# Optimization experiments

Hardware: AMD Instinct MI355X
Metric: run time of the kernel (lower is better)

The kernel has to match this reference:

```python
import jax, jax.numpy as jnp
import numpy as np

H = 8          # num_heads
D = 64         # out_dim per head
ROT = D // 2   # rotary dim per spatial axis (out_dim // relative_emb_dim)
MIN_FREQ = 1.0 / 64


def _freqs(t):
    # t: (bs, N) coordinates -> (bs, N, ROT)
    inv_freq = 1.0 / (10000.0 ** (jnp.arange(0, ROT, 2, dtype=jnp.float32) / ROT))
    f = (t / MIN_FREQ)[..., None] * inv_freq  # (bs, N, ROT/2)
    return jnp.concatenate([f, f], axis=-1)   # (bs, N, ROT)


def _rotate_half(x):
    x1, x2 = jnp.split(x, 2, axis=-1)
    return jnp.concatenate([-x2, x1], axis=-1)


def _rope(t, f):
    return t * jnp.cos(f) + _rotate_half(t) * jnp.sin(f)


def reference(h, pos, Wq, Wk, Wv, src, dst):
    bs, N, _ = pos.shape
    hb = h.reshape(bs, N, -1)                       # (bs, N, C)
    # Faithful to torch: Linear output (bs,N,H*D) .view(bs,H,N,D) is a raw
    # memory reinterpretation, i.e. a reshape, not a transpose.
    Qh = (hb @ Wq.T).reshape(bs, H, N, D)
    Kh = (hb @ Wk.T).reshape(bs, H, N, D)
    Vh = (hb @ Wv.T).reshape(bs, H, N, D)

    fx = _freqs(pos[..., 0])[:, None]               # (bs, 1, N, ROT) broadcast over heads
    fy = _freqs(pos[..., 1])[:, None]

    def rope2d(t):
        return jnp.concatenate([_rope(t[..., :ROT], fx), _rope(t[..., ROT:], fy)], axis=-1)

    Qh = rope2d(Qh)
    Kh = rope2d(Kh)

    Qn = Qh.reshape(-1, H, D)                       # (bs*N, H, D) flat node layout
    Kn = Kh.reshape(-1, H, D)
    Vn = Vh.reshape(-1, H, D)

    # edge attention: gather, dot, clamped exp, scatter-sum
    score = jnp.sum(Kn[src] * Qn[dst], axis=-1)     # (E, H)
    score = jnp.exp(jnp.clip(score / np.sqrt(D).astype(np.float32), -5.0, 5.0))

    nseg = bs * N
    wV = jax.ops.segment_sum(Vn[src] * score[..., None], dst, num_segments=nseg)  # (nseg,H,D)
    z = jax.ops.segment_sum(score, dst, num_segments=nseg)                        # (nseg,H)

    attn_out = wV / z[..., None]
    return attn_out.reshape(-1, H * D)


def setup_inputs() -> dict:
    key = jax.random.key(0)
    k = jax.random.split(key, 7)
    bs, N, C, E = 4, 4096, 256, 524288
    return {
        "h": jax.random.normal(k[0], (bs * N, C), dtype=jnp.float32),
        "pos": jax.random.uniform(k[1], (bs, N, 2), dtype=jnp.float32),
        "Wq": jax.random.normal(k[2], (H * D, C), dtype=jnp.float32) * 0.05,
        "Wk": jax.random.normal(k[3], (H * D, C), dtype=jnp.float32) * 0.05,
        "Wv": jax.random.normal(k[4], (H * D, C), dtype=jnp.float32) * 0.05,
        "src": jax.random.randint(k[5], (E,), 0, bs * N, dtype=jnp.int32),
        "dst": jax.random.randint(k[6], (E,), 0, bs * N, dtype=jnp.int32),
    }
```

## Files before the change

kernel.cpp:

```cpp
#include <hip/hip_runtime.h>
#include <math.h>

#define NODES 16384
#define CIN   256
#define HD    512
#define NPOS  4096
#define NHEAD 8
#define DDIM  64
#define HN    (NODES * CIN)
#define WN    (HD * CIN)

typedef float f32x4 __attribute__((ext_vector_type(4)));
typedef unsigned int u32x4 __attribute__((ext_vector_type(4)));
typedef short s16x8 __attribute__((ext_vector_type(8)));

__device__ inline unsigned short f2bf(float f) {
  unsigned int u = __float_as_uint(f);
  u += 0x7fffu + ((u >> 16) & 1u);
  return (unsigned short)(u >> 16);
}

__global__ __launch_bounds__(256) void conv_kernel(
    const float* __restrict__ h, const float* __restrict__ wq,
    const float* __restrict__ wk, const float* __restrict__ wv,
    unsigned short* __restrict__ out) {
  size_t e = ((size_t)blockIdx.x * 256 + threadIdx.x) * 8;
  const float* s;
  size_t off;
  if (e < HN)               { s = h;  off = e; }
  else if (e < HN + WN)     { s = wq; off = e - HN; }
  else if (e < HN + 2 * WN) { s = wk; off = e - HN - WN; }
  else                      { s = wv; off = e - HN - 2 * WN; }
  float4 f0 = *(const float4*)(s + off);
  float4 f1 = *(const float4*)(s + off + 4);
  u32x4 o;
  o[0] = f2bf(f0.x) | ((unsigned int)f2bf(f0.y) << 16);
  o[1] = f2bf(f0.z) | ((unsigned int)f2bf(f0.w) << 16);
  o[2] = f2bf(f1.x) | ((unsigned int)f2bf(f1.y) << 16);
  o[3] = f2bf(f1.z) | ((unsigned int)f2bf(f1.w) << 16);
  *(u32x4*)(out + e) = o;
}

__global__ __launch_bounds__(256) void gemm_mfma_kernel(
    const unsigned short* __restrict__ hb,
    const unsigned short* __restrict__ wb,
    unsigned short* __restrict__ Qb, unsigned short* __restrict__ Kb,
    unsigned short* __restrict__ Vb) {
  const unsigned short* B = wb + (size_t)blockIdx.z * WN;
  unsigned short* C = blockIdx.z == 0 ? Qb : (blockIdx.z == 1 ? Kb : Vb);

  __shared__ __align__(16) unsigned short As[2][128 * 32];
  __shared__ __align__(16) unsigned short Bs[2][128 * 32];

  const int tid = threadIdx.x;
  const int lane = tid & 63, w = tid >> 6;
  const int row0 = blockIdx.y * 128, col0 = blockIdx.x * 128;
  const int wr = w >> 1, wc = w & 1;

  const int r_l = lane >> 2;
  const int kc = (lane & 3) * 8;

  f32x4 acc[4][4] = {};

#define STAGE(bufi, kt)                                                        \
  {                                                                            \
    _Pragma("unroll") for (int u = 0; u < 2; ++u) {                            \
      int blk = u * 4 + w;                                                     \
      int r = blk * 16 + r_l;                                                  \
      __builtin_amdgcn_global_load_lds(                                        \
          (const __attribute__((address_space(1))) void*)(hb +                 \
              (size_t)(row0 + r) * CIN + (kt) + kc),                           \
          (__attribute__((address_space(3))) void*)(&As[bufi][blk * 512]),     \
          16, 0, 0);                                                           \
      __builtin_amdgcn_global_load_lds(                                        \
          (const __attribute__((address_space(1))) void*)(B +                  \
              (size_t)(col0 + r) * CIN + (kt) + kc),                           \
          (__attribute__((address_space(3))) void*)(&Bs[bufi][blk * 512]),     \
          16, 0, 0);                                                           \
    }                                                                          \
  }

  STAGE(0, 0);
  __syncthreads();

  int cur = 0;
  for (int t = 0; t < 8; ++t) {
    if (t < 7) STAGE(cur ^ 1, (t + 1) * 32);

    s16x8 af[4], bfr[4];
#pragma unroll
    for (int mi = 0; mi < 4; ++mi)
      af[mi] = *(const s16x8*)(&As[cur][(wr * 64 + mi * 16 + (lane & 15)) * 32 + (lane >> 4) * 8]);
#pragma unroll
    for (int ni = 0; ni < 4; ++ni)
      bfr[ni] = *(const s16x8*)(&Bs[cur][(wc * 64 + ni * 16 + (lane & 15)) * 32 + (lane >> 4) * 8]);
#pragma unroll
    for (int mi = 0; mi < 4; ++mi)
#pragma unroll
      for (int ni = 0; ni < 4; ++ni)
        acc[mi][ni] = __builtin_amdgcn_mfma_f32_16x16x32_bf16(
            af[mi], bfr[ni], acc[mi][ni], 0, 0, 0);

    __syncthreads();
    cur ^= 1;
  }
#undef STAGE

#pragma unroll
  for (int mi = 0; mi < 4; ++mi) {
    int rbase = row0 + wr * 64 + mi * 16 + (lane >> 4) * 4;
#pragma unroll
    for (int ni = 0; ni < 4; ++ni) {
      int c = col0 + wc * 64 + ni * 16 + (lane & 15);
#pragma unroll
      for (int r = 0; r < 4; ++r)
        C[(size_t)(rbase + r) * HD + c] = f2bf(acc[mi][ni][r]);
    }
  }
}

__global__ __launch_bounds__(256) void rope_kernel(
    unsigned short* __restrict__ Qb, unsigned short* __restrict__ Kb,
    const float* __restrict__ pos) {
  const float INVF[16] = {
      1.0f, 0.5623413252f, 0.3162277660f, 0.1778279410f,
      0.1f, 0.05623413252f, 0.03162277660f, 0.01778279410f,
      0.01f, 0.005623413252f, 0.003162277660f, 0.001778279410f,
      0.001f, 0.0005623413252f, 0.0003162277660f, 0.0001778279410f};
  int t = blockIdx.x * 256 + threadIdx.x;
  unsigned short* M = (t >> 18) ? Kb : Qb;
  int p = t & ((1 << 18) - 1);
  int rem = p >> 1, q = p & 1;
  int n = rem & (NPOS - 1);
  int b = rem >> 15;
  float ps = pos[((size_t)((b << 12) + n)) * 2 + q] * 64.0f;

  unsigned short* base = M + (size_t)rem * DDIM + q * 32;
  u32x4 lo0 = *(u32x4*)(base);
  u32x4 lo1 = *(u32x4*)(base + 8);
  u32x4 hi0 = *(u32x4*)(base + 16);
  u32x4 hi1 = *(u32x4*)(base + 24);
  float lo[16], hi[16];
#pragma unroll
  for (int j = 0; j < 4; ++j) {
    lo[2 * j]     = __uint_as_float(lo0[j] << 16);
    lo[2 * j + 1] = __uint_as_float(lo0[j] & 0xffff0000u);
    lo[8 + 2 * j]     = __uint_as_float(lo1[j] << 16);
    lo[8 + 2 * j + 1] = __uint_as_float(lo1[j] & 0xffff0000u);
    hi[2 * j]     = __uint_as_float(hi0[j] << 16);
    hi[2 * j + 1] = __uint_as_float(hi0[j] & 0xffff0000u);
    hi[8 + 2 * j]     = __uint_as_float(hi1[j] << 16);
    hi[8 + 2 * j + 1] = __uint_as_float(hi1[j] & 0xffff0000u);
  }
  unsigned short o[32];
#pragma unroll
  for (int i = 0; i < 16; ++i) {
    float s, c;
    sincosf(ps * INVF[i], &s, &c);
    o[i]      = f2bf(lo[i] * c - hi[i] * s);
    o[i + 16] = f2bf(hi[i] * c + lo[i] * s);
  }
  u32x4 ov;
#pragma unroll
  for (int blkk = 0; blkk < 4; ++blkk) {
#pragma unroll
    for (int j = 0; j < 4; ++j)
      ov[j] = (unsigned int)o[blkk * 8 + 2 * j] |
              ((unsigned int)o[blkk * 8 + 2 * j + 1] << 16);
    *(u32x4*)(base + blkk * 8) = ov;
  }
}

__global__ __launch_bounds__(256) void hist_kernel(
    const int* __restrict__ dst, int* __restrict__ count, int E) {
  int t = blockIdx.x * 256 + threadIdx.x;
  if (t < E) atomicAdd(&count[dst[t]], 1);
}

__global__ __launch_bounds__(256) void scan_kernel(
    const int* __restrict__ count, int* __restrict__ offset,
    int* __restrict__ cursor) {
  __shared__ int psum[256];
  __shared__ int pref[256];
  int t = threadIdx.x;
  int base = t * (NODES / 256);
  int s = 0;
  for (int i = 0; i < NODES / 256; ++i) s += count[base + i];
  psum[t] = s;
  __syncthreads();
  if (t == 0) {
    int run = 0;
    for (int i = 0; i < 256; ++i) { pref[i] = run; run += psum[i]; }
  }
  __syncthreads();
  int off = pref[t];
  for (int i = 0; i < NODES / 256; ++i) {
    int c = count[base + i];
    offset[base + i] = off;
    cursor[base + i] = off;
    off += c;
  }
  if (t == 255) offset[NODES] = off;
}

__global__ __launch_bounds__(256) void scatter_kernel(
    const int* __restrict__ src, const int* __restrict__ dst,
    int* __restrict__ cursor, int* __restrict__ srcs, int E) {
  int t = blockIdx.x * 256 + threadIdx.x;
  if (t < E) {
    int p = atomicAdd(&cursor[dst[t]], 1);
    srcs[p] = src[t];
  }
}

__global__ __launch_bounds__(256) void node_kernel(
    const unsigned short* __restrict__ Qb, const unsigned short* __restrict__ Kb,
    const unsigned short* __restrict__ Vb,
    const int* __restrict__ srcs, const int* __restrict__ offset,
    float* __restrict__ out) {
  __shared__ float wv[4][HD];
  __shared__ float zb[4][NHEAD];
  const int n = blockIdx.x;
  const int tid = threadIdx.x;
  const int lane = tid & 63, w = tid >> 6;
  const int hh = lane >> 3, g = lane & 7;

  const int beg = offset[n], end = offset[n + 1];

  u32x4 qu = *(const u32x4*)(Qb + (size_t)n * HD + lane * 8);
  float qf[8];
#pragma unroll
  for (int j = 0; j < 4; ++j) {
    qf[2 * j]     = __uint_as_float(qu[j] << 16);
    qf[2 * j + 1] = __uint_as_float(qu[j] & 0xffff0000u);
  }

  float a[8] = {0, 0, 0, 0, 0, 0, 0, 0};
  float zacc = 0.f;

  int i = beg + w;
  for (; i + 4 < end; i += 8) {
    int s0 = srcs[i];
    int s1 = srcs[i + 4];
    u32x4 ku0 = *(const u32x4*)(Kb + (size_t)s0 * HD + lane * 8);
    u32x4 ku1 = *(const u32x4*)(Kb + (size_t)s1 * HD + lane * 8);
    u32x4 vu0 = *(const u32x4*)(Vb + (size_t)s0 * HD + lane * 8);
    u32x4 vu1 = *(const u32x4*)(Vb + (size_t)s1 * HD + lane * 8);
    float dot0 = 0.f, dot1 = 0.f;
#pragma unroll
    for (int j = 0; j < 4; ++j) {
      dot0 += __uint_as_float(ku0[j] << 16) * qf[2 * j];
      dot0 += __uint_as_float(ku0[j] & 0xffff0000u) * qf[2 * j + 1];
      dot1 += __uint_as_float(ku1[j] << 16) * qf[2 * j];
      dot1 += __uint_as_float(ku1[j] & 0xffff0000u) * qf[2 * j + 1];
    }
    dot0 += __shfl_xor(dot0, 1);
    dot1 += __shfl_xor(dot1, 1);
    dot0 += __shfl_xor(dot0, 2);
    dot1 += __shfl_xor(dot1, 2);
    dot0 += __shfl_xor(dot0, 4);
    dot1 += __shfl_xor(dot1, 4);
    float sc0 = expf(fminf(fmaxf(dot0 * 0.125f, -5.0f), 5.0f));
    float sc1 = expf(fminf(fmaxf(dot1 * 0.125f, -5.0f), 5.0f));
#pragma unroll
    for (int j = 0; j < 4; ++j) {
      a[2 * j]     += __uint_as_float(vu0[j] << 16) * sc0 +
                      __uint_as_float(vu1[j] << 16) * sc1;
      a[2 * j + 1] += __uint_as_float(vu0[j] & 0xffff0000u) * sc0 +
                      __uint_as_float(vu1[j] & 0xffff0000u) * sc1;
    }
    zacc += sc0 + sc1;
  }
  for (; i < end; i += 4) {
    int s = srcs[i];
    u32x4 ku = *(const u32x4*)(Kb + (size_t)s * HD + lane * 8);
    u32x4 vu = *(const u32x4*)(Vb + (size_t)s * HD + lane * 8);
    float dot = 0.f;
#pragma unroll
    for (int j = 0; j < 4; ++j) {
      dot += __uint_as_float(ku[j] << 16) * qf[2 * j];
      dot += __uint_as_float(ku[j] & 0xffff0000u) * qf[2 * j + 1];
    }
    dot += __shfl_xor(dot, 1);
    dot += __shfl_xor(dot, 2);
    dot += __shfl_xor(dot, 4);
    float sc = expf(fminf(fmaxf(dot * 0.125f, -5.0f), 5.0f));
#pragma unroll
    for (int j = 0; j < 4; ++j) {
      a[2 * j]     += __uint_as_float(vu[j] << 16) * sc;
      a[2 * j + 1] += __uint_as_float(vu[j] & 0xffff0000u) * sc;
    }
    zacc += sc;
  }

  *(float4*)&wv[w][lane * 8]     = make_float4(a[0], a[1], a[2], a[3]);
  *(float4*)&wv[w][lane * 8 + 4] = make_float4(a[4], a[5], a[6], a[7]);
  if (g == 0) zb[w][hh] = zacc;
  __syncthreads();

  const int d0 = tid * 2;
  float r0 = wv[0][d0] + wv[1][d0] + wv[2][d0] + wv[3][d0];
  float r1 = wv[0][d0 + 1] + wv[1][d0 + 1] + wv[2][d0 + 1] + wv[3][d0 + 1];
  const int head = d0 >> 6;
  float zz = zb[0][head] + zb[1][head] + zb[2][head] + zb[3][head];
  float inv = 1.0f / zz;
  *(float2*)&out[(size_t)n * HD + d0] = make_float2(r0 * inv, r1 * inv);
}

extern "C" void kernel_launch(void* const* d_in, const int* in_sizes, int n_in,
                              void* d_out, int out_size, void* d_ws,
                              size_t ws_size, hipStream_t stream) {
  const float* h   = (const float*)d_in[0];
  const float* pos = (const float*)d_in[1];
  const float* Wq  = (const float*)d_in[2];
  const float* Wk  = (const float*)d_in[3];
  const float* Wv  = (const float*)d_in[4];
  const int* src   = (const int*)d_in[5];
  const int* dst   = (const int*)d_in[6];
  const int E = in_sizes[5];

  unsigned short* hb  = (unsigned short*)d_ws;
  unsigned short* wb  = hb + HN;
  unsigned short* Qb  = wb + 3 * WN;
  unsigned short* Kb  = Qb + (size_t)NODES * HD;
  unsigned short* Vb  = Kb + (size_t)NODES * HD;
  int* count  = (int*)(Vb + (size_t)NODES * HD);
  int* offset = count + NODES;
  int* cursor = offset + NODES + 1;
  int* srcs   = cursor + NODES;
  float* out = (float*)d_out;

  hipMemsetAsync(count, 0, NODES * sizeof(int), stream);

  conv_kernel<<<(HN + 3 * WN) / 8 / 256, 256, 0, stream>>>(h, Wq, Wk, Wv, hb);

  gemm_mfma_kernel<<<dim3(HD / 128, NODES / 128, 3), 256, 0, stream>>>(
      hb, wb, Qb, Kb, Vb);

  rope_kernel<<<(2 * 131072 * 2) / 256, 256, 0, stream>>>(Qb, Kb, pos);

  hist_kernel<<<(E + 255) / 256, 256, 0, stream>>>(dst, count, E);
  scan_kernel<<<1, 256, 0, stream>>>(count, offset, cursor);
  scatter_kernel<<<(E + 255) / 256, 256, 0, stream>>>(src, dst, cursor, srcs, E);

  node_kernel<<<NODES, 256, 0, stream>>>(Qb, Kb, Vb, srcs, offset, out);
}
```

Baseline: 320.4 us.

## Fuse RoPE into GEMM epilogue and histogram into conversion kernel

Applies the 2D rotary embedding directly in the GEMM epilogue on fp32 accumulators, dropping the separate rope kernel and its read-modify-write pass over Q and K. Folds the dst histogram into the bf16 conversion kernel, whose grid covers more threads than there are edges, and reorders launches so the CSR build runs before the GEMM. It also removes the 2-edge unrolled loop in the node kernel in favour of the simple single-edge loop. In exchange the epilogue computes sincos per element with per-row pos loads, and the node kernel loses memory-level parallelism from the unroll.

```diff
diff --git a/kernel.cpp b/kernel.cpp
--- a/kernel.cpp
+++ b/kernel.cpp
@@ -20,11 +20,15 @@
   return (unsigned short)(u >> 16);
 }
 
-__global__ __launch_bounds__(256) void conv_kernel(
+__global__ __launch_bounds__(256) void conv_hist_kernel(
     const float* __restrict__ h, const float* __restrict__ wq,
     const float* __restrict__ wk, const float* __restrict__ wv,
-    unsigned short* __restrict__ out) {
-  size_t e = ((size_t)blockIdx.x * 256 + threadIdx.x) * 8;
+    unsigned short* __restrict__ out,
+    const int* __restrict__ dst, int* __restrict__ count, int E) {
+  int t = blockIdx.x * 256 + threadIdx.x;
+  if (t < E) atomicAdd(&count[dst[t]], 1);
+
+  size_t e = (size_t)t * 8;
   const float* s;
   size_t off;
   if (e < HN)               { s = h;  off = e; }
@@ -44,10 +48,12 @@
 __global__ __launch_bounds__(256) void gemm_mfma_kernel(
     const unsigned short* __restrict__ hb,
     const unsigned short* __restrict__ wb,
+    const float* __restrict__ pos,
     unsigned short* __restrict__ Qb, unsigned short* __restrict__ Kb,
     unsigned short* __restrict__ Vb) {
-  const unsigned short* B = wb + (size_t)blockIdx.z * WN;
-  unsigned short* C = blockIdx.z == 0 ? Qb : (blockIdx.z == 1 ? Kb : Vb);
+  const int z = blockIdx.z;
+  const unsigned short* B = wb + (size_t)z * WN;
+  unsigned short* C = z == 0 ? Qb : (z == 1 ? Kb : Vb);
 
   __shared__ __align__(16) unsigned short As[2][128 * 32];
   __shared__ __align__(16) unsigned short Bs[2][128 * 32];
@@ -106,75 +112,40 @@
   }
 #undef STAGE
 
+  const int head = blockIdx.x * 2 + wc;
+  const int cb = col0 + wc * 64 + (lane & 15);
+  const float invf = exp2f(-(float)(lane & 15) * 0.83048202372184f);
+
 #pragma unroll
   for (int mi = 0; mi < 4; ++mi) {
-    int rbase = row0 + wr * 64 + mi * 16 + (lane >> 4) * 4;
-#pragma unroll
-    for (int ni = 0; ni < 4; ++ni) {
-      int c = col0 + wc * 64 + ni * 16 + (lane & 15);
-#pragma unroll
-      for (int r = 0; r < 4; ++r)
-        C[(size_t)(rbase + r) * HD + c] = f2bf(acc[mi][ni][r]);
+#pragma unroll
+    for (int r = 0; r < 4; ++r) {
+      int row = row0 + wr * 64 + mi * 16 + (lane >> 4) * 4 + r;
+      float v0 = acc[mi][0][r], v1 = acc[mi][1][r];
+      float v2 = acc[mi][2][r], v3 = acc[mi][3][r];
+      if (z < 2) {
+        int b = row >> 12;
+        int rem = ((row & 4095) << 3) + head;
+        int n = rem & (NPOS - 1);
+        const float* pp = pos + ((size_t)((b << 12) + n)) * 2;
+        float a0 = pp[0] * 64.0f * invf;
+        float a1 = pp[1] * 64.0f * invf;
+        float s0, c0, s1, c1;
+        sincosf(a0, &s0, &c0);
+        sincosf(a1, &s1, &c1);
+        float nx0 = v0 * c0 - v1 * s0;
+        float nx1 = v1 * c0 + v0 * s0;
+        float ny0 = v2 * c1 - v3 * s1;
+        float ny1 = v3 * c1 + v2 * s1;
+        v0 = nx0; v1 = nx1; v2 = ny0; v3 = ny1;
+      }
+      unsigned short* cp = C + (size_t)row * HD + cb;
+      cp[0]  = f2bf(v0);
+      cp[16] = f2bf(v1);
+      cp[32] = f2bf(v2);
+      cp[48] = f2bf(v3);
     }
   }
-}
-
-__global__ __launch_bounds__(256) void rope_kernel(
-    unsigned short* __restrict__ Qb, unsigned short* __restrict__ Kb,
-    const float* __restrict__ pos) {
-  const float INVF[16] = {
-      1.0f, 0.5623413252f, 0.3162277660f, 0.1778279410f,
-      0.1f, 0.05623413252f, 0.03162277660f, 0.01778279410f,
-      0.01f, 0.005623413252f, 0.003162277660f, 0.001778279410f,
-      0.001f, 0.0005623413252f, 0.0003162277660f, 0.0001778279410f};
-  int t = blockIdx.x * 256 + threadIdx.x;
-  unsigned short* M = (t >> 18) ? Kb : Qb;
-  int p = t & ((1 << 18) - 1);
-  int rem = p >> 1, q = p & 1;
-  int n = rem & (NPOS - 1);
-  int b = rem >> 15;
-  float ps = pos[((size_t)((b << 12) + n)) * 2 + q] * 64.0f;
-
-  unsigned short* base = M + (size_t)rem * DDIM + q * 32;
-  u32x4 lo0 = *(u32x4*)(base);
-  u32x4 lo1 = *(u32x4*)(base + 8);
-  u32x4 hi0 = *(u32x4*)(base + 16);
-  u32x4 hi1 = *(u32x4*)(base + 24);
-  float lo[16], hi[16];
-#pragma unroll
-  for (int j = 0; j < 4; ++j) {
-    lo[2 * j]     = __uint_as_float(lo0[j] << 16);
-    lo[2 * j + 1] = __uint_as_float(lo0[j] & 0xffff0000u);
-    lo[8 + 2 * j]     = __uint_as_float(lo1[j] << 16);
-    lo[8 + 2 * j + 1] = __uint_as_float(lo1[j] & 0xffff0000u);
-    hi[2 * j]     = __uint_as_float(hi0[j] << 16);
-    hi[2 * j + 1] = __uint_as_float(hi0[j] & 0xffff0000u);
-    hi[8 + 2 * j]     = __uint_as_float(hi1[j] << 16);
-    hi[8 + 2 * j + 1] = __uint_as_float(hi1[j] & 0xffff0000u);
-  }
-  unsigned short o[32];
-#pragma unroll
-  for (int i = 0; i < 16; ++i) {
-    float s, c;
-    sincosf(ps * INVF[i], &s, &c);
-    o[i]      = f2bf(lo[i] * c - hi[i] * s);
-    o[i + 16] = f2bf(hi[i] * c + lo[i] * s);
-  }
-  u32x4 ov;
-#pragma unroll
-  for (int blkk = 0; blkk < 4; ++blkk) {
-#pragma unroll
-    for (int j = 0; j < 4; ++j)
-      ov[j] = (unsigned int)o[blkk * 8 + 2 * j] |
-              ((unsigned int)o[blkk * 8 + 2 * j + 1] << 16);
-    *(u32x4*)(base + blkk * 8) = ov;
-  }
-}
-
-__global__ __launch_bounds__(256) void hist_kernel(
-    const int* __restrict__ dst, int* __restrict__ count, int E) {
-  int t = blockIdx.x * 256 + threadIdx.x;
-  if (t < E) atomicAdd(&count[dst[t]], 1);
 }
 
 __global__ __launch_bounds__(256) void scan_kernel(
@@ -238,40 +209,7 @@
   float a[8] = {0, 0, 0, 0, 0, 0, 0, 0};
   float zacc = 0.f;
 
-  int i = beg + w;
-  for (; i + 4 < end; i += 8) {
-    int s0 = srcs[i];
-    int s1 = srcs[i + 4];
-    u32x4 ku0 = *(const u32x4*)(Kb + (size_t)s0 * HD + lane * 8);
-    u32x4 ku1 = *(const u32x4*)(Kb + (size_t)s1 * HD + lane * 8);
-    u32x4 vu0 = *(const u32x4*)(Vb + (size_t)s0 * HD + lane * 8);
-    u32x4 vu1 = *(const u32x4*)(Vb + (size_t)s1 * HD + lane * 8);
-    float dot0 = 0.f, dot1 = 0.f;
-#pragma unroll
-    for (int j = 0; j < 4; ++j) {
-      dot0 += __uint_as_float(ku0[j] << 16) * qf[2 * j];
-      dot0 += __uint_as_float(ku0[j] & 0xffff0000u) * qf[2 * j + 1];
-      dot1 += __uint_as_float(ku1[j] << 16) * qf[2 * j];
-      dot1 += __uint_as_float(ku1[j] & 0xffff0000u) * qf[2 * j + 1];
-    }
-    dot0 += __shfl_xor(dot0, 1);
-    dot1 += __shfl_xor(dot1, 1);
-    dot0 += __shfl_xor(dot0, 2);
-    dot1 += __shfl_xor(dot1, 2);
-    dot0 += __shfl_xor(dot0, 4);
-    dot1 += __shfl_xor(dot1, 4);
-    float sc0 = expf(fminf(fmaxf(dot0 * 0.125f, -5.0f), 5.0f));
-    float sc1 = expf(fminf(fmaxf(dot1 * 0.125f, -5.0f), 5.0f));
-#pragma unroll
-    for (int j = 0; j < 4; ++j) {
-      a[2 * j]     += __uint_as_float(vu0[j] << 16) * sc0 +
-                      __uint_as_float(vu1[j] << 16) * sc1;
-      a[2 * j + 1] += __uint_as_float(vu0[j] & 0xffff0000u) * sc0 +
-                      __uint_as_float(vu1[j] & 0xffff0000u) * sc1;
-    }
-    zacc += sc0 + sc1;
-  }
-  for (; i < end; i += 4) {
+  for (int i = beg + w; i < end; i += 4) {
     int s = srcs[i];
     u32x4 ku = *(const u32x4*)(Kb + (size_t)s * HD + lane * 8);
     u32x4 vu = *(const u32x4*)(Vb + (size_t)s * HD + lane * 8);
@@ -332,16 +270,14 @@
 
   hipMemsetAsync(count, 0, NODES * sizeof(int), stream);
 
-  conv_kernel<<<(HN + 3 * WN) / 8 / 256, 256, 0, stream>>>(h, Wq, Wk, Wv, hb);
-
-  gemm_mfma_kernel<<<dim3(HD / 128, NODES / 128, 3), 256, 0, stream>>>(
-      hb, wb, Qb, Kb, Vb);
-
-  rope_kernel<<<(2 * 131072 * 2) / 256, 256, 0, stream>>>(Qb, Kb, pos);
-
-  hist_kernel<<<(E + 255) / 256, 256, 0, stream>>>(dst, count, E);
+  conv_hist_kernel<<<(HN + 3 * WN) / 8 / 256, 256, 0, stream>>>(
+      h, Wq, Wk, Wv, hb, dst, count, E);
+
   scan_kernel<<<1, 256, 0, stream>>>(count, offset, cursor);
   scatter_kernel<<<(E + 255) / 256, 256, 0, stream>>>(src, dst, cursor, srcs, E);
 
+  gemm_mfma_kernel<<<dim3(HD / 128, NODES / 128, 3), 256, 0, stream>>>(
+      hb, wb, pos, Qb, Kb, Vb);
+
   node_kernel<<<NODES, 256, 0, stream>>>(Qb, Kb, Vb, srcs, offset, out);
 }
```

Measured after the change: 308.0 us. 3.9% less time.
